# Kernel tuning notes

Hardware: AMD Instinct MI355X
Metric: run time of the kernel (lower is better)

The kernel has to match this reference:

```python
import jax, jax.numpy as jnp
import numpy as np

N = 4_000_000
H, W = 1080, 1920


def setup_inputs() -> dict:
    key = jax.random.key(0)
    ks = jax.random.split(key, 4)
    # points mostly in front of the camera (viewmat = identity)
    means = jax.random.normal(ks[0], (N, 3), jnp.float32) * jnp.array([2.0, 2.0, 1.5], jnp.float32) + jnp.array([0.0, 0.0, 5.0], jnp.float32)
    colors = jax.random.normal(ks[1], (N, 3), jnp.float32)          # pre-sigmoid logits
    opacities = jax.random.normal(ks[2], (N, 1), jnp.float32)       # pre-sigmoid logits (unused by solid rasterizer)
    scales = jax.random.normal(ks[3], (N, 3), jnp.float32) * 0.1 - 5.0
    quats = jnp.concatenate([jnp.ones((N, 1), jnp.float32), jnp.zeros((N, 3), jnp.float32)], axis=1)
    viewmat = jnp.eye(4, dtype=jnp.float32)
    K = jnp.array([[1000.0, 0.0, W / 2.0], [0.0, 1000.0, H / 2.0], [0.0, 0.0, 1.0]], jnp.float32)
    return dict(means=means, colors=colors, opacities=opacities, scales=scales,
                quats=quats, viewmat=viewmat, K=K, height=H, width=W)


def _rasterize_solid(means, colors, viewmat, K, height, width):
    # camera transform
    R = viewmat[:3, :3]
    t = viewmat[:3, 3]
    mc = means @ R.T + t                     # [N,3] points in camera frame
    z = mc[:, 2]
    front = z > 0.1
    z_safe = jnp.where(front, z, 1.0)        # avoid div-by-~0 for culled points
    fx, fy, cx, cy = K[0, 0], K[1, 1], K[0, 2], K[1, 2]
    x = mc[:, 0] * fx / z_safe + cx
    y = mc[:, 1] * fy / z_safe + cy
    on = front & (x >= 0) & (x < width - 1) & (y >= 0) & (y < height - 1)

    x0f = jnp.floor(x)
    y0f = jnp.floor(y)
    dx = x - x0f
    dy = y - y0f
    x0 = jnp.clip(x0f.astype(jnp.int32), 0, width - 1)
    y0 = jnp.clip(y0f.astype(jnp.int32), 0, height - 1)
    x1 = jnp.clip(x0 + 1, 0, width - 1)
    y1 = jnp.clip(y0 + 1, 0, height - 1)
    pix = y0 * width + x0

    # scatter-min reproduces that order-independently. Off points contribute +inf.
    zbuf = jnp.full((height * width,), jnp.inf, means.dtype).at[pix].min(jnp.where(on, z, jnp.inf))
    zbuf = jax.lax.stop_gradient(zbuf)       # only feeds a boolean test, no grad path in torch either
    vis = on & (z <= zbuf[pix] + 0.05)
    visf = vis.astype(means.dtype)

    # bilinear weights; (wb <-> y1x0, wc <-> y0x1) pairing kept faithful to source
    wa = (1 - dx) * (1 - dy) * visf
    wb = dx * (1 - dy) * visf
    wc = (1 - dx) * dy * visf
    wd = dx * dy * visf

    feat = jnp.concatenate([colors, z[:, None]], axis=1)   # [N,4] rgb+depth
    buf = jnp.zeros((height * width, 5), means.dtype)
    for idx, w in ((pix, wa), (y1 * width + x0, wb), (y0 * width + x1, wc), (y1 * width + x1, wd)):
        buf = buf.at[idx].add(jnp.concatenate([feat * w[:, None], w[:, None]], axis=1))

    total = buf[:, 4:5] + 1e-6
    ff = buf[:, 0:4] / total
    rgb = jnp.clip(ff[:, 0:3], 0.0, 1.0)
    return jnp.concatenate([rgb, ff[:, 3:4]], axis=1).reshape(height, width, 4)


def reference(means, colors, opacities, scales, quats, viewmat, K, height, width):
    render_colors = jax.nn.sigmoid(colors)
    _ = jax.nn.sigmoid(opacities)  # computed in torch forward, unused by solid rasterizer
    return _rasterize_solid(means, render_colors, viewmat, K, height, width)
```

## Files before the change

### kernel.cpp

```cpp
#include <hip/hip_runtime.h>
#include <math.h>

#define IMG_H 1080
#define IMG_W 1920
#define NPIX (IMG_H * IMG_W)

#define TILE_W 64
#define TILE_H 8
#define NTX (IMG_W / TILE_W)
#define NTY (IMG_H / TILE_H)
#define NTILES (NTX * NTY)
#define TPIX (TILE_W * TILE_H)

#define NSEG 256
#define SEGT 1024

#define ZMW (TILE_W + 1)
#define ZMH (TILE_H + 1)
#define ZMN (ZMW * ZMH)

#define CAP 2048

__device__ __attribute__((noinline)) float4 project4(
    const float* __restrict__ vm, const float* __restrict__ Km,
    float mx, float my, float mz)
{
    float mcx = vm[0] * mx + vm[1] * my + vm[2]  * mz + vm[3];
    float mcy = vm[4] * mx + vm[5] * my + vm[6]  * mz + vm[7];
    float mcz = vm[8] * mx + vm[9] * my + vm[10] * mz + vm[11];
    float z = mcz;
    bool front = z > 0.1f;
    float z_safe = front ? z : 1.0f;
    float x = mcx * Km[0] / z_safe + Km[2];
    float y = mcy * Km[4] / z_safe + Km[5];
    return make_float4(x, y, z, front ? 1.0f : 0.0f);
}

__device__ __forceinline__ bool on_test(const float4& p)
{
    return (p.w != 0.0f) && (p.x >= 0.0f) && (p.x < (float)(IMG_W - 1))
                         && (p.y >= 0.0f) && (p.y < (float)(IMG_H - 1));
}

__device__ __forceinline__ void project_pt(
    const float* __restrict__ vm, const float* __restrict__ Km,
    float mx, float my, float mz,
    float& x, float& y, float& z, bool& on)
{
    float mcx = vm[0] * mx + vm[1] * my + vm[2]  * mz + vm[3];
    float mcy = vm[4] * mx + vm[5] * my + vm[6]  * mz + vm[7];
    float mcz = vm[8] * mx + vm[9] * my + vm[10] * mz + vm[11];
    z = mcz;
    bool front = z > 0.1f;
    float z_safe = front ? z : 1.0f;
    x = mcx * Km[0] / z_safe + Km[2];
    y = mcy * Km[4] / z_safe + Km[5];
    on = front && (x >= 0.0f) && (x < (float)(IMG_W - 1))
               && (y >= 0.0f) && (y < (float)(IMG_H - 1));
}

__global__ __launch_bounds__(SEGT) void k_count(
    const float* __restrict__ means, const float* __restrict__ vm,
    const float* __restrict__ Km, unsigned int* __restrict__ hist,
    int N, int C)
{
    __shared__ unsigned int h[NTILES];
    int tid = threadIdx.x, w = blockIdx.x;
    for (int t = tid; t < NTILES; t += SEGT) h[t] = 0u;
    __syncthreads();
    int start = w * C, end = min(start + C, N);
    for (int j = start + tid; j < end; j += SEGT) {
        float4 p = project4(vm, Km, means[3 * j], means[3 * j + 1], means[3 * j + 2]);
        if (!on_test(p)) continue;
        int x0 = (int)floorf(p.x), y0 = (int)floorf(p.y);
        int tx0 = x0 >> 6, ty0 = y0 >> 3;
        int tx1 = (x0 + 1) >> 6, ty1 = (y0 + 1) >> 3;
#pragma unroll
        for (int sy = 0; sy < 2; ++sy) {
            int ty = sy ? ty1 : ty0;
            if (sy && ty1 == ty0) continue;
#pragma unroll
            for (int sx = 0; sx < 2; ++sx) {
                int tx = sx ? tx1 : tx0;
                if (sx && tx1 == tx0) continue;
                atomicAdd(&h[ty * NTX + tx], 1u);
            }
        }
    }
    __syncthreads();
    for (int t = tid; t < NTILES; t += SEGT)
        hist[(size_t)w * NTILES + t] = h[t];
}

__global__ __launch_bounds__(256) void k_colpref(
    const unsigned int* __restrict__ hist, unsigned int* __restrict__ histBase,
    unsigned int* __restrict__ tileBase)
{
    int t = blockIdx.x * 256 + threadIdx.x;
    if (t >= NTILES) return;
    unsigned int run = 0u;
#pragma unroll 4
    for (int w = 0; w < NSEG; ++w) {
        unsigned int v = hist[(size_t)w * NTILES + t];
        histBase[(size_t)w * NTILES + t] = run;
        run += v;
    }
    tileBase[t] = run;
}

__global__ __launch_bounds__(256) void k_scan(unsigned int* __restrict__ tileBase)
{
    __shared__ unsigned int part[256];
    int tid = threadIdx.x;
    unsigned int loc[16];
    unsigned int sum = 0u;
#pragma unroll
    for (int i = 0; i < 16; ++i) {
        int t = tid * 16 + i;
        unsigned int v = (t < NTILES) ? tileBase[t] : 0u;
        loc[i] = sum;
        sum += v;
    }
    part[tid] = sum;
    __syncthreads();
    if (tid == 0) {
        unsigned int run = 0u;
        for (int i = 0; i < 256; ++i) {
            unsigned int v = part[i];
            part[i] = run;
            run += v;
        }
        tileBase[NTILES] = run;
    }
    __syncthreads();
    unsigned int base = part[tid];
#pragma unroll
    for (int i = 0; i < 16; ++i) {
        int t = tid * 16 + i;
        if (t < NTILES) tileBase[t] = base + loc[i];
    }
}

__global__ __launch_bounds__(SEGT) void k_binscatter(
    const float* __restrict__ means, const float* __restrict__ colors,
    const float* __restrict__ vm, const float* __restrict__ Km,
    const unsigned int* __restrict__ histBase,
    const unsigned int* __restrict__ tileBase,
    float4* __restrict__ records, int N, int C, unsigned int cap)
{
    __shared__ unsigned int cur[NTILES];
    int tid = threadIdx.x, w = blockIdx.x;
    for (int t = tid; t < NTILES; t += SEGT)
        cur[t] = tileBase[t] + histBase[(size_t)w * NTILES + t];
    __syncthreads();
    int start = w * C, end = min(start + C, N);
    for (int j = start + tid; j < end; j += SEGT) {
        float4 p = project4(vm, Km, means[3 * j], means[3 * j + 1], means[3 * j + 2]);
        if (!on_test(p)) continue;
        float r = 1.0f / (1.0f + expf(-colors[3 * j]));
        float g = 1.0f / (1.0f + expf(-colors[3 * j + 1]));
        float b = 1.0f / (1.0f + expf(-colors[3 * j + 2]));
        unsigned int ri = (unsigned int)(r * 1023.0f + 0.5f);
        unsigned int gi = (unsigned int)(g * 1023.0f + 0.5f);
        unsigned int bi = (unsigned int)(b * 1023.0f + 0.5f);
        float4 rec = make_float4(p.x, p.y, p.z,
                                 __uint_as_float(ri | (gi << 10) | (bi << 20)));
        int x0 = (int)floorf(p.x), y0 = (int)floorf(p.y);
        int tx0 = x0 >> 6, ty0 = y0 >> 3;
        int tx1 = (x0 + 1) >> 6, ty1 = (y0 + 1) >> 3;
#pragma unroll
        for (int sy = 0; sy < 2; ++sy) {
            int ty = sy ? ty1 : ty0;
            if (sy && ty1 == ty0) continue;
#pragma unroll
            for (int sx = 0; sx < 2; ++sx) {
                int tx = sx ? tx1 : tx0;
                if (sx && tx1 == tx0) continue;
                int t = ty * NTX + tx;
                unsigned int slot = atomicAdd(&cur[t], 1u);
                if (slot < cap) records[slot] = rec;
            }
        }
    }
}

__global__ __launch_bounds__(256) void k_tile_pre16(
    const unsigned int* __restrict__ tileBase,
    const float4* __restrict__ records, float* __restrict__ out,
    unsigned int cap)
{
    __shared__ float sR[TPIX], sG[TPIX], sB[TPIX], sZ[TPIX], sW[TPIX];
    __shared__ unsigned int sZmin[ZMN];
    int tid = threadIdx.x;
    int t = blockIdx.x;
    int txb = (t % NTX) * TILE_W;
    int tyb = (t / NTX) * TILE_H;
    for (int p = tid; p < TPIX; p += 256) {
        sR[p] = 0.0f; sG[p] = 0.0f; sB[p] = 0.0f; sZ[p] = 0.0f; sW[p] = 0.0f;
    }
    for (int p = tid; p < ZMN; p += 256) sZmin[p] = 0x7F800000u;
    __syncthreads();

    unsigned int base = tileBase[t], next = tileBase[t + 1];
    int cnt = 0;
    if (base < cap) cnt = (int)min(next - base, cap - base);
    const float4* rec = records + base;

    for (int j = tid; j < cnt; j += 256) {
        float4 v = rec[j];
        int x0l = (int)floorf(v.x) - txb;
        int y0l = (int)floorf(v.y) - tyb;
        atomicMin(&sZmin[(y0l + 1) * ZMW + (x0l + 1)], __float_as_uint(v.z));
    }
    __syncthreads();

    for (int j = tid; j < cnt; j += 256) {
        float4 v = rec[j];
        float x = v.x, y = v.y, z = v.z;
        float x0f = floorf(x), y0f = floorf(y);
        int x0l = (int)x0f - txb, y0l = (int)y0f - tyb;
        float zmin = __uint_as_float(sZmin[(y0l + 1) * ZMW + (x0l + 1)]);
        if (!(z <= zmin + 0.05f)) continue;
        unsigned int rgb = __float_as_uint(v.w);
        float r = (float)(rgb & 1023u) * (1.0f / 1023.0f);
        float g = (float)((rgb >> 10) & 1023u) * (1.0f / 1023.0f);
        float b = (float)((rgb >> 20) & 1023u) * (1.0f / 1023.0f);
        float dx = x - x0f, dy = y - y0f;
        float wa = (1.0f - dx) * (1.0f - dy);
        float wb = dx * (1.0f - dy);
        float wc = (1.0f - dx) * dy;
        float wd = dx * dy;
        int cxs[4] = { x0l, x0l, x0l + 1, x0l + 1 };
        int cys[4] = { y0l, y0l + 1, y0l, y0l + 1 };
        float ws[4] = { wa, wb, wc, wd };
#pragma unroll
        for (int c = 0; c < 4; ++c) {
            int lx = cxs[c], ly = cys[c];
            if ((unsigned)lx < TILE_W && (unsigned)ly < TILE_H) {
                int lp = ly * TILE_W + lx;
                float w = ws[c];
                atomicAdd(&sR[lp], r * w);
                atomicAdd(&sG[lp], g * w);
                atomicAdd(&sB[lp], b * w);
                atomicAdd(&sZ[lp], z * w);
                atomicAdd(&sW[lp], w);
            }
        }
    }
    __syncthreads();

    for (int p = tid; p < TPIX; p += 256) {
        float tot = sW[p] + 1e-6f;
        float r = sR[p] / tot, g = sG[p] / tot, b = sB[p] / tot, zz = sZ[p] / tot;
        r = fminf(fmaxf(r, 0.0f), 1.0f);
        g = fminf(fmaxf(g, 0.0f), 1.0f);
        b = fminf(fmaxf(b, 0.0f), 1.0f);
        int gy = tyb + p / TILE_W, gx = txb + p % TILE_W;
        reinterpret_cast<float4*>(out)[gy * IMG_W + gx] = make_float4(r, g, b, zz);
    }
}


__global__ __launch_bounds__(256) void k_zmin(
    const float* __restrict__ means, const float* __restrict__ vm,
    const float* __restrict__ Km, unsigned int* __restrict__ zbuf, int N)
{
    int i = blockIdx.x * 256 + threadIdx.x;
    if (i >= N) return;
    float x, y, z; bool on;
    project_pt(vm, Km, means[3 * i], means[3 * i + 1], means[3 * i + 2], x, y, z, on);
    if (!on) return;
    int x0 = (int)floorf(x), y0 = (int)floorf(y);
    atomicMin(&zbuf[y0 * IMG_W + x0], __float_as_uint(z));
}

__global__ __launch_bounds__(256) void k_scatter_u32(
    const float* __restrict__ means, const float* __restrict__ vm,
    const float* __restrict__ Km, const unsigned int* __restrict__ zbuf,
    unsigned int* __restrict__ cursors, unsigned int* __restrict__ records, int N)
{
    int i = blockIdx.x * 256 + threadIdx.x;
    if (i >= N) return;
    float x, y, z; bool on;
    project_pt(vm, Km, means[3 * i], means[3 * i + 1], means[3 * i + 2], x, y, z, on);
    if (!on) return;
    int x0 = (int)floorf(x), y0 = (int)floorf(y);
    int pix = y0 * IMG_W + x0;
    if (!(z <= __uint_as_float(zbuf[pix]) + 0.05f)) return;
    int tx0 = x0 / TILE_W, ty0 = y0 / TILE_H;
    int tx1 = (x0 + 1) / TILE_W, ty1 = (y0 + 1) / TILE_H;
#pragma unroll
    for (int sy = 0; sy < 2; ++sy) {
        int ty = sy ? ty1 : ty0;
        if (sy && ty1 == ty0) continue;
#pragma unroll
        for (int sx = 0; sx < 2; ++sx) {
            int tx = sx ? tx1 : tx0;
            if (sx && tx1 == tx0) continue;
            int t = ty * NTX + tx;
            unsigned int slot = atomicAdd(&cursors[t], 1u);
            if (slot < CAP) records[(size_t)t * CAP + slot] = (unsigned int)i;
        }
    }
}

__global__ __launch_bounds__(256) void k_tile_u32(
    const float* __restrict__ means, const float* __restrict__ colors,
    const float* __restrict__ vm, const float* __restrict__ Km,
    const unsigned int* __restrict__ cursors,
    const unsigned int* __restrict__ records,
    float* __restrict__ out)
{
    __shared__ float sR[TPIX], sG[TPIX], sB[TPIX], sZ[TPIX], sW[TPIX];
    int tid = threadIdx.x;
    int t = blockIdx.x;
    int txb = (t % NTX) * TILE_W;
    int tyb = (t / NTX) * TILE_H;
    for (int p = tid; p < TPIX; p += 256) {
        sR[p] = 0.0f; sG[p] = 0.0f; sB[p] = 0.0f; sZ[p] = 0.0f; sW[p] = 0.0f;
    }
    __syncthreads();

    int cnt = (int)min(cursors[t], (unsigned int)CAP);
    const unsigned int* rec = records + (size_t)t * CAP;
    for (int j = tid; j < cnt; j += 256) {
        int i = (int)rec[j];
        float x, y, z; bool on;
        project_pt(vm, Km, means[3 * i], means[3 * i + 1], means[3 * i + 2], x, y, z, on);
        float x0f = floorf(x), y0f = floorf(y);
        int x0 = (int)x0f, y0 = (int)y0f;
        float dx = x - x0f, dy = y - y0f;
        float wa = (1.0f - dx) * (1.0f - dy);
        float wb = dx * (1.0f - dy);
        float wc = (1.0f - dx) * dy;
        float wd = dx * dy;
        float r = 1.0f / (1.0f + expf(-colors[3 * i]));
        float g = 1.0f / (1.0f + expf(-colors[3 * i + 1]));
        float b = 1.0f / (1.0f + expf(-colors[3 * i + 2]));
        int cxs[4] = { x0, x0, x0 + 1, x0 + 1 };
        int cys[4] = { y0, y0 + 1, y0, y0 + 1 };
        float ws[4] = { wa, wb, wc, wd };
#pragma unroll
        for (int c = 0; c < 4; ++c) {
            int lx = cxs[c] - txb, ly = cys[c] - tyb;
            if ((unsigned)lx < TILE_W && (unsigned)ly < TILE_H) {
                int lp = ly * TILE_W + lx;
                float w = ws[c];
                atomicAdd(&sR[lp], r * w);
                atomicAdd(&sG[lp], g * w);
                atomicAdd(&sB[lp], b * w);
                atomicAdd(&sZ[lp], z * w);
                atomicAdd(&sW[lp], w);
            }
        }
    }
    __syncthreads();

    for (int p = tid; p < TPIX; p += 256) {
        float tot = sW[p] + 1e-6f;
        float r = sR[p] / tot, g = sG[p] / tot, b = sB[p] / tot, zz = sZ[p] / tot;
        r = fminf(fmaxf(r, 0.0f), 1.0f);
        g = fminf(fmaxf(g, 0.0f), 1.0f);
        b = fminf(fmaxf(b, 0.0f), 1.0f);
        int gy = tyb + p / TILE_W, gx = txb + p % TILE_W;
        reinterpret_cast<float4*>(out)[gy * IMG_W + gx] = make_float4(r, g, b, zz);
    }
}


__global__ __launch_bounds__(256) void k_splat(
    const float* __restrict__ means, const float* __restrict__ colors,
    const float* __restrict__ vm, const float* __restrict__ Km,
    const float* __restrict__ zbuf,
    float* __restrict__ acc, float* __restrict__ wsum, int N)
{
    int i = blockIdx.x * 256 + threadIdx.x;
    if (i >= N) return;
    float x, y, z; bool on;
    project_pt(vm, Km, means[3 * i], means[3 * i + 1], means[3 * i + 2], x, y, z, on);
    if (!on) return;
    float x0f = floorf(x), y0f = floorf(y);
    int x0 = (int)x0f, y0 = (int)y0f;
    int pix = y0 * IMG_W + x0;
    if (!(z <= zbuf[pix] + 0.05f)) return;
    float dx = x - x0f, dy = y - y0f;
    float wa = (1.0f - dx) * (1.0f - dy);
    float wb = dx * (1.0f - dy);
    float wc = (1.0f - dx) * dy;
    float wd = dx * dy;
    float r = 1.0f / (1.0f + expf(-colors[3 * i]));
    float g = 1.0f / (1.0f + expf(-colors[3 * i + 1]));
    float b = 1.0f / (1.0f + expf(-colors[3 * i + 2]));
    int ia = pix, ib = pix + IMG_W, ic = pix + 1, id = pix + IMG_W + 1;
#define SPLAT1(idx, w)                                    \
    do {                                                  \
        atomicAdd(&acc[4 * (idx) + 0], r * (w));          \
        atomicAdd(&acc[4 * (idx) + 1], g * (w));          \
        atomicAdd(&acc[4 * (idx) + 2], b * (w));          \
        atomicAdd(&acc[4 * (idx) + 3], z * (w));          \
        atomicAdd(&wsum[(idx)], (w));                     \
    } while (0)
    SPLAT1(ia, wa); SPLAT1(ib, wb); SPLAT1(ic, wc); SPLAT1(id, wd);
#undef SPLAT1
}

__global__ __launch_bounds__(256) void k_final(
    float* __restrict__ out, const float* __restrict__ wsum)
{
    int p = blockIdx.x * 256 + threadIdx.x;
    if (p >= NPIX) return;
    float tot = wsum[p] + 1e-6f;
    float4 v = reinterpret_cast<float4*>(out)[p];
    float r = v.x / tot, g = v.y / tot, b = v.z / tot, zz = v.w / tot;
    r = fminf(fmaxf(r, 0.0f), 1.0f);
    g = fminf(fmaxf(g, 0.0f), 1.0f);
    b = fminf(fmaxf(b, 0.0f), 1.0f);
    reinterpret_cast<float4*>(out)[p] = make_float4(r, g, b, zz);
}

extern "C" void kernel_launch(void* const* d_in, const int* in_sizes, int n_in,
                              void* d_out, int out_size, void* d_ws, size_t ws_size,
                              hipStream_t stream)
{
    const float* means  = (const float*)d_in[0];
    const float* colors = (const float*)d_in[1];
    const float* vm     = (const float*)d_in[5];
    const float* Km     = (const float*)d_in[6];
    int N = in_sizes[0] / 3;
    float* out = (float*)d_out;

    const size_t histB   = (size_t)NSEG * NTILES * 4;
    const size_t tbB     = (size_t)(NTILES + 1) * 4;
    size_t fixedA        = 2 * histB + tbB;
    fixedA               = (fixedA + 15) & ~(size_t)15;
    const size_t zbufB   = (size_t)NPIX * 4;
    const size_t curB    = (size_t)NTILES * 4;
    const size_t recU32B = (size_t)NTILES * CAP * 4;

    if (ws_size >= fixedA + ((size_t)128 << 20)) {
        unsigned int* hist     = (unsigned int*)d_ws;
        unsigned int* histBase = (unsigned int*)((char*)d_ws + histB);
        unsigned int* tileBase = (unsigned int*)((char*)d_ws + 2 * histB);
        float4*       records  = (float4*)((char*)d_ws + fixedA);
        unsigned int  cap      = (unsigned int)min((ws_size - fixedA) / 16,
                                                   (size_t)0x0FFFFFFF);
        int C = (N + NSEG - 1) / NSEG;
        k_count     <<<NSEG, SEGT, 0, stream>>>(means, vm, Km, hist, N, C);
        k_colpref   <<<(NTILES + 255) / 256, 256, 0, stream>>>(hist, histBase,
                                                               tileBase);
        k_scan      <<<1, 256, 0, stream>>>(tileBase);
        k_binscatter<<<NSEG, SEGT, 0, stream>>>(means, colors, vm, Km,
                                                histBase, tileBase, records,
                                                N, C, cap);
        k_tile_pre16<<<NTILES, 256, 0, stream>>>(tileBase, records, out, cap);
    } else if (ws_size >= zbufB + curB + recU32B) {
        unsigned int* zbuf    = (unsigned int*)d_ws;
        unsigned int* cursors = (unsigned int*)((char*)d_ws + zbufB);
        unsigned int* records = (unsigned int*)((char*)d_ws + zbufB + curB);
        int nb = (N + 255) / 256;
        hipMemsetAsync(zbuf, 0x7f, zbufB, stream);
        hipMemsetAsync(cursors, 0, curB, stream);
        k_zmin       <<<nb, 256, 0, stream>>>(means, vm, Km, zbuf, N);
        k_scatter_u32<<<nb, 256, 0, stream>>>(means, vm, Km, zbuf, cursors,
                                              records, N);
        k_tile_u32   <<<NTILES, 256, 0, stream>>>(means, colors, vm, Km,
                                                  cursors, records, out);
    } else {
        unsigned int* zbuf = (unsigned int*)d_ws;
        float*        wsum = (float*)((char*)d_ws + zbufB);
        int nb = (N + 255) / 256;
        hipMemsetAsync(zbuf, 0x7f, zbufB, stream);
        hipMemsetAsync(wsum, 0x00, zbufB, stream);
        hipMemsetAsync(out,  0x00, (size_t)NPIX * 16, stream);
        k_zmin <<<nb, 256, 0, stream>>>(means, vm, Km, zbuf, N);
        k_splat<<<nb, 256, 0, stream>>>(means, colors, vm, Km,
                                        (const float*)zbuf, out, wsum, N);
        k_final<<<(NPIX + 255) / 256, 256, 0, stream>>>(out, wsum);
    }
}
```

Before: 474.5 us.

## Replace per-tile shared-atomic splatting with counting sort and per-pixel gather

The tile kernel now counting-sorts each tile's records by their base pixel bin into a shared index list. It computes each bin's min depth by scanning that bin's list, then has each output pixel gather from its four neighbouring bins and accumulate in registers. This removes the five shared-memory float atomics per corner per point and the separate min-depth atomic pass. In exchange it adds a block-wide scan and re-reads records from global memory through the index list. Records per tile are capped at 4096, so very dense tiles could silently drop points. The number of histogram segments is also doubled and the prefix loop unroll raised.

```diff
diff --git a/kernel.cpp b/kernel.cpp
--- a/kernel.cpp
+++ b/kernel.cpp
@@ -12,13 +12,14 @@
 #define NTILES (NTX * NTY)
 #define TPIX (TILE_W * TILE_H)
 
-#define NSEG 256
+#define NSEG 512
 #define SEGT 1024
 
 #define ZMW (TILE_W + 1)
 #define ZMH (TILE_H + 1)
-#define ZMN (ZMW * ZMH)
-
+#define NBIN (ZMW * ZMH)
+
+#define CAPT 4096
 #define CAP 2048
 
 __device__ __attribute__((noinline)) float4 project4(
@@ -99,7 +100,7 @@
     int t = blockIdx.x * 256 + threadIdx.x;
     if (t >= NTILES) return;
     unsigned int run = 0u;
-#pragma unroll 4
+#pragma unroll 8
     for (int w = 0; w < NSEG; ++w) {
         unsigned int v = hist[(size_t)w * NTILES + t];
         histBase[(size_t)w * NTILES + t] = run;
@@ -184,79 +185,118 @@
     }
 }
 
-__global__ __launch_bounds__(256) void k_tile_pre16(
+__global__ __launch_bounds__(256) void k_tile_sort(
     const unsigned int* __restrict__ tileBase,
     const float4* __restrict__ records, float* __restrict__ out,
     unsigned int cap)
 {
-    __shared__ float sR[TPIX], sG[TPIX], sB[TPIX], sZ[TPIX], sW[TPIX];
-    __shared__ unsigned int sZmin[ZMN];
+    __shared__ unsigned short sIdx[CAPT];
+    __shared__ int sStart[NBIN + 1];
+    __shared__ int sCur[NBIN];
+    __shared__ float sZmin[NBIN];
+    __shared__ int sScan[256];
+
     int tid = threadIdx.x;
     int t = blockIdx.x;
     int txb = (t % NTX) * TILE_W;
     int tyb = (t / NTX) * TILE_H;
-    for (int p = tid; p < TPIX; p += 256) {
-        sR[p] = 0.0f; sG[p] = 0.0f; sB[p] = 0.0f; sZ[p] = 0.0f; sW[p] = 0.0f;
-    }
-    for (int p = tid; p < ZMN; p += 256) sZmin[p] = 0x7F800000u;
-    __syncthreads();
 
     unsigned int base = tileBase[t], next = tileBase[t + 1];
     int cnt = 0;
-    if (base < cap) cnt = (int)min(next - base, cap - base);
+    if (base < cap) cnt = (int)min(min(next - base, cap - base), (unsigned int)CAPT);
     const float4* rec = records + base;
 
-    for (int j = tid; j < cnt; j += 256) {
-        float4 v = rec[j];
-        int x0l = (int)floorf(v.x) - txb;
-        int y0l = (int)floorf(v.y) - tyb;
-        atomicMin(&sZmin[(y0l + 1) * ZMW + (x0l + 1)], __float_as_uint(v.z));
-    }
-    __syncthreads();
-
-    for (int j = tid; j < cnt; j += 256) {
-        float4 v = rec[j];
-        float x = v.x, y = v.y, z = v.z;
-        float x0f = floorf(x), y0f = floorf(y);
-        int x0l = (int)x0f - txb, y0l = (int)y0f - tyb;
-        float zmin = __uint_as_float(sZmin[(y0l + 1) * ZMW + (x0l + 1)]);
-        if (!(z <= zmin + 0.05f)) continue;
-        unsigned int rgb = __float_as_uint(v.w);
-        float r = (float)(rgb & 1023u) * (1.0f / 1023.0f);
-        float g = (float)((rgb >> 10) & 1023u) * (1.0f / 1023.0f);
-        float b = (float)((rgb >> 20) & 1023u) * (1.0f / 1023.0f);
-        float dx = x - x0f, dy = y - y0f;
-        float wa = (1.0f - dx) * (1.0f - dy);
-        float wb = dx * (1.0f - dy);
-        float wc = (1.0f - dx) * dy;
-        float wd = dx * dy;
-        int cxs[4] = { x0l, x0l, x0l + 1, x0l + 1 };
-        int cys[4] = { y0l, y0l + 1, y0l, y0l + 1 };
-        float ws[4] = { wa, wb, wc, wd };
+    for (int b = tid; b < NBIN; b += 256) sCur[b] = 0;
+    __syncthreads();
+
+    int hb[16];
+#pragma unroll
+    for (int u = 0; u < 16; ++u) {
+        int j = tid + u * 256;
+        hb[u] = -1;
+        if (j < cnt) {
+            float4 v = rec[j];
+            int x0l = (int)floorf(v.x) - txb;
+            int y0l = (int)floorf(v.y) - tyb;
+            int b = (y0l + 1) * ZMW + (x0l + 1);
+            hb[u] = b;
+            atomicAdd(&sCur[b], 1);
+        }
+    }
+    __syncthreads();
+
+    int b0 = tid * 3;
+    int c0 = (b0     < NBIN) ? sCur[b0]     : 0;
+    int c1 = (b0 + 1 < NBIN) ? sCur[b0 + 1] : 0;
+    int c2 = (b0 + 2 < NBIN) ? sCur[b0 + 2] : 0;
+    int local = c0 + c1 + c2;
+    sScan[tid] = local;
+    __syncthreads();
+    for (int off = 1; off < 256; off <<= 1) {
+        int v = (tid >= off) ? sScan[tid - off] : 0;
+        __syncthreads();
+        sScan[tid] += v;
+        __syncthreads();
+    }
+    int run = sScan[tid] - local;
+    if (b0 < NBIN)     { sStart[b0]     = run;           sCur[b0]     = run; }
+    if (b0 + 1 < NBIN) { sStart[b0 + 1] = run + c0;      sCur[b0 + 1] = run + c0; }
+    if (b0 + 2 < NBIN) { sStart[b0 + 2] = run + c0 + c1; sCur[b0 + 2] = run + c0 + c1; }
+    if (tid == 255) sStart[NBIN] = cnt;
+    __syncthreads();
+
+#pragma unroll
+    for (int u = 0; u < 16; ++u) {
+        if (hb[u] >= 0) {
+            int j = tid + u * 256;
+            int slot = atomicAdd(&sCur[hb[u]], 1);
+            sIdx[slot] = (unsigned short)j;
+        }
+    }
+    __syncthreads();
+
+    for (int b = tid; b < NBIN; b += 256) {
+        float zm = 1e30f;
+        int e = sStart[b + 1];
+        for (int k = sStart[b]; k < e; ++k)
+            zm = fminf(zm, rec[sIdx[k]].z);
+        sZmin[b] = zm;
+    }
+    __syncthreads();
+
+    for (int p = tid; p < TPIX; p += 256) {
+        int px = p % TILE_W, py = p / TILE_W;
+        float ra = 0.0f, ga = 0.0f, ba = 0.0f, za = 0.0f, wsum = 0.0f;
 #pragma unroll
         for (int c = 0; c < 4; ++c) {
-            int lx = cxs[c], ly = cys[c];
-            if ((unsigned)lx < TILE_W && (unsigned)ly < TILE_H) {
-                int lp = ly * TILE_W + lx;
-                float w = ws[c];
-                atomicAdd(&sR[lp], r * w);
-                atomicAdd(&sG[lp], g * w);
-                atomicAdd(&sB[lp], b * w);
-                atomicAdd(&sZ[lp], z * w);
-                atomicAdd(&sW[lp], w);
+            int ox = c & 1, oy = c >> 1;
+            int hx = px - ox, hy = py - oy;
+            int b = (hy + 1) * ZMW + (hx + 1);
+            float zlim = sZmin[b] + 0.05f;
+            int e = sStart[b + 1];
+            for (int k = sStart[b]; k < e; ++k) {
+                float4 v = rec[sIdx[k]];
+                if (!(v.z <= zlim)) continue;
+                float dx = v.x - floorf(v.x);
+                float dy = v.y - floorf(v.y);
+                float wgt = (oy ? dx : (1.0f - dx)) * (ox ? dy : (1.0f - dy));
+                unsigned int rgb = __float_as_uint(v.w);
+                ra += (float)(rgb & 1023u) * wgt;
+                ga += (float)((rgb >> 10) & 1023u) * wgt;
+                ba += (float)((rgb >> 20) & 1023u) * wgt;
+                za += v.z * wgt;
+                wsum += wgt;
             }
         }
-    }
-    __syncthreads();
-
-    for (int p = tid; p < TPIX; p += 256) {
-        float tot = sW[p] + 1e-6f;
-        float r = sR[p] / tot, g = sG[p] / tot, b = sB[p] / tot, zz = sZ[p] / tot;
-        r = fminf(fmaxf(r, 0.0f), 1.0f);
-        g = fminf(fmaxf(g, 0.0f), 1.0f);
-        b = fminf(fmaxf(b, 0.0f), 1.0f);
-        int gy = tyb + p / TILE_W, gx = txb + p % TILE_W;
-        reinterpret_cast<float4*>(out)[gy * IMG_W + gx] = make_float4(r, g, b, zz);
+        float tot = wsum + 1e-6f;
+        float inv = (1.0f / 1023.0f) / tot;
+        float r = ra * inv, g = ga * inv, b2 = ba * inv;
+        float zz = za / tot;
+        r  = fminf(fmaxf(r, 0.0f), 1.0f);
+        g  = fminf(fmaxf(g, 0.0f), 1.0f);
+        b2 = fminf(fmaxf(b2, 0.0f), 1.0f);
+        int gy = tyb + py, gx = txb + px;
+        reinterpret_cast<float4*>(out)[gy * IMG_W + gx] = make_float4(r, g, b2, zz);
     }
 }
 
@@ -452,7 +492,7 @@
         k_binscatter<<<NSEG, SEGT, 0, stream>>>(means, colors, vm, Km,
                                                 histBase, tileBase, records,
                                                 N, C, cap);
-        k_tile_pre16<<<NTILES, 256, 0, stream>>>(tileBase, records, out, cap);
+        k_tile_sort <<<NTILES, 256, 0, stream>>>(tileBase, records, out, cap);
     } else if (ws_size >= zbufB + curB + recU32B) {
         unsigned int* zbuf    = (unsigned int*)d_ws;
         unsigned int* cursors = (unsigned int*)((char*)d_ws + zbufB);
```

New measurement: 419.9 us. -11.5%, faster.
